# Performance work log

Measured on AMD Instinct MI355X. Metric: run time of the kernel, lower is better.

## Reference

```python
import jax, jax.numpy as jnp
import numpy as np

CONTEXT_SIZE = 2048
CONTEXT_DIM = 1024
HIDDEN_SIZE = 1024
BATCH = 32
SEQLEN = 64


def setup_inputs() -> dict:
    key = jax.random.key(0)
    k1, k2, k3 = jax.random.split(key, 3)
    hidden = jax.random.normal(k1, (1, BATCH, HIDDEN_SIZE), dtype=jnp.float32)
    contextvects = jax.random.normal(k2, (CONTEXT_SIZE, BATCH, CONTEXT_DIM), dtype=jnp.float32)
    # nn.Linear weight: [out_features=context_dim, in_features=hidden_size]
    W = jax.random.normal(k3, (CONTEXT_DIM, HIDDEN_SIZE), dtype=jnp.float32) / np.sqrt(HIDDEN_SIZE)
    padding_mask = jnp.zeros((CONTEXT_SIZE, BATCH), dtype=bool)
    return {"seqlen": SEQLEN, "hidden": hidden, "contextvects": contextvects,
            "W": W, "padding_mask": padding_mask}


def reference(seqlen, hidden, contextvects, W, padding_mask):
    # hidden: [1, B, H] -> [B, H]
    h = hidden[0]
    # Linear projection (no bias): [B, D]
    hidden_proj = h @ W.T
    # scores over context positions: [C, B]
    scores = jnp.einsum('cbd,bd->cb', contextvects, hidden_proj)
    scores = jnp.where(padding_mask, -jnp.inf, scores)
    # softmax over context dim (dim=0)
    attn_weights = jax.nn.softmax(scores, axis=0)  # [C, B]
    # weighted sum of context vectors: [B, D]
    ctx = jnp.einsum('cb,cbd->bd', attn_weights, contextvects)
    # the torch loop recomputes identical values for every step -> broadcast
    context = jnp.broadcast_to(ctx[None], (seqlen, ctx.shape[0], ctx.shape[1]))
    attentions = jnp.broadcast_to(attn_weights.T[None],
                                  (seqlen, attn_weights.shape[1], attn_weights.shape[0]))
    return context, attentions
```

## Files before the change

### kernel.cpp

```cpp
#include <hip/hip_runtime.h>
#include <math.h>

#define C_SIZE 2048
#define D_DIM  1024
#define H_DIM  1024
#define B_SIZE 32
#define S_LEN  64
#define G_NUM  32
#define CG     (C_SIZE / G_NUM)

__global__ __launch_bounds__(256) void hp_kernel(const float* __restrict__ hidden,
                                                 const float* __restrict__ W,
                                                 float* __restrict__ hp) {
    int b    = blockIdx.x;
    int dg   = blockIdx.y;
    int lane = threadIdx.x & 63;
    int wave = threadIdx.x >> 6;

    const float* hrow = hidden + b * H_DIM;
    float4 h4[4];
#pragma unroll
    for (int k = 0; k < 4; ++k) h4[k] = *(const float4*)(hrow + k * 256 + 4 * lane);

    const int d0 = dg * 32 + wave * 8;
    const float* wp = W + (size_t)d0 * H_DIM + 4 * lane;
    float4 wb[2][4];
#pragma unroll
    for (int k = 0; k < 4; ++k) wb[0][k] = *(const float4*)(wp + k * 256);

#pragma unroll
    for (int i = 0; i < 8; ++i) {
        if (i < 7) {
            const float* wn = wp + (size_t)(i + 1) * H_DIM;
#pragma unroll
            for (int k = 0; k < 4; ++k) wb[(i + 1) & 1][k] = *(const float4*)(wn + k * 256);
        }
        float s = 0.f;
#pragma unroll
        for (int k = 0; k < 4; ++k) {
            float4 w4 = wb[i & 1][k];
            s += w4.x * h4[k].x + w4.y * h4[k].y + w4.z * h4[k].z + w4.w * h4[k].w;
        }
        for (int off = 32; off > 0; off >>= 1) s += __shfl_xor(s, off);
        if (lane == 0) hp[b * D_DIM + d0 + i] = s;
    }
}

__global__ __launch_bounds__(256, 4) void fused_kernel(const float* __restrict__ cv,
                                                       const float* __restrict__ hp,
                                                       const unsigned char* __restrict__ mask,
                                                       float* __restrict__ scoresT,
                                                       float* __restrict__ pm,
                                                       float* __restrict__ pl,
                                                       float* __restrict__ pacc) {
    int g    = blockIdx.x;
    int b    = blockIdx.y;
    int lane = threadIdx.x & 63;
    int wave = threadIdx.x >> 6;

    const float* hpb = hp + b * D_DIM;
    float4 hp4[4];
#pragma unroll
    for (int k = 0; k < 4; ++k) hp4[k] = *(const float4*)(hpb + k * 256 + 4 * lane);

    const int    c0      = g * CG + wave * (CG / 4);
    const size_t cstride = (size_t)B_SIZE * D_DIM;
    const float* p0      = cv + ((size_t)c0 * B_SIZE + b) * D_DIM + 4 * lane;

    int mreg = 0;
    if (lane < 16) mreg = mask[(size_t)(c0 + lane) * B_SIZE + b];

    float  m = -3.0e38f, l = 0.f;
    float  myscore = 0.f;
    float4 acc[4];
#pragma unroll
    for (int k = 0; k < 4; ++k) acc[k] = make_float4(0.f, 0.f, 0.f, 0.f);

    float4 buf[2][4];
#pragma unroll
    for (int k = 0; k < 4; ++k) buf[0][k] = *(const float4*)(p0 + k * 256);
#pragma unroll
    for (int k = 0; k < 4; ++k) buf[1][k] = *(const float4*)(p0 + cstride + k * 256);

#pragma unroll
    for (int i = 0; i < 16; ++i) {
        float4 cvv[4];
#pragma unroll
        for (int k = 0; k < 4; ++k) cvv[k] = buf[i & 1][k];

        if (i < 14) {
            const float* pn = p0 + (size_t)(i + 2) * cstride;
#pragma unroll
            for (int k = 0; k < 4; ++k) buf[i & 1][k] = *(const float4*)(pn + k * 256);
        }

        float s = 0.f;
#pragma unroll
        for (int k = 0; k < 4; ++k) {
            s += cvv[k].x * hp4[k].x + cvv[k].y * hp4[k].y +
                 cvv[k].z * hp4[k].z + cvv[k].w * hp4[k].w;
        }
        for (int off = 32; off > 0; off >>= 1) s += __shfl_xor(s, off);

        if (__shfl(mreg, i, 64)) s = -3.0e38f;
        if (lane == i) myscore = s;

        if (s <= m) {
            float p = __expf(s - m);
            l += p;
#pragma unroll
            for (int k = 0; k < 4; ++k) {
                acc[k].x += p * cvv[k].x;
                acc[k].y += p * cvv[k].y;
                acc[k].z += p * cvv[k].z;
                acc[k].w += p * cvv[k].w;
            }
        } else {
            float scale = __expf(m - s);
            l = l * scale + 1.f;
#pragma unroll
            for (int k = 0; k < 4; ++k) {
                acc[k].x = acc[k].x * scale + cvv[k].x;
                acc[k].y = acc[k].y * scale + cvv[k].y;
                acc[k].z = acc[k].z * scale + cvv[k].z;
                acc[k].w = acc[k].w * scale + cvv[k].w;
            }
            m = s;
        }
    }

    if (lane < 16) scoresT[b * C_SIZE + c0 + lane] = myscore;

    __shared__ float sm[4], sl[4];
    __shared__ float accs[4][D_DIM];
    if (lane == 0) { sm[wave] = m; sl[wave] = l; }
    __syncthreads();

    float mb = fmaxf(fmaxf(sm[0], sm[1]), fmaxf(sm[2], sm[3]));
    float myscale = __expf(m - mb);
#pragma unroll
    for (int k = 0; k < 4; ++k) {
        float4 v = acc[k];
        v.x *= myscale; v.y *= myscale; v.z *= myscale; v.w *= myscale;
        *(float4*)&accs[wave][k * 256 + 4 * lane] = v;
    }
    float lb = 0.f;
#pragma unroll
    for (int w = 0; w < 4; ++w) lb += sl[w] * __expf(sm[w] - mb);
    __syncthreads();

    int t = threadIdx.x;
    float4 r = make_float4(0.f, 0.f, 0.f, 0.f);
#pragma unroll
    for (int w = 0; w < 4; ++w) {
        float4 v = *(const float4*)&accs[w][t * 4];
        r.x += v.x; r.y += v.y; r.z += v.z; r.w += v.w;
    }
    *(float4*)(pacc + ((size_t)g * B_SIZE + b) * D_DIM + t * 4) = r;
    if (t == 0) { pm[g * B_SIZE + b] = mb; pl[g * B_SIZE + b] = lb; }
}

__global__ __launch_bounds__(64) void ctx_kernel(const float* __restrict__ pm,
                                                 const float* __restrict__ pl,
                                                 const float* __restrict__ pacc,
                                                 float* __restrict__ Mb,
                                                 float* __restrict__ Lb,
                                                 float* __restrict__ ctxws) {
    int b     = blockIdx.x;
    int dbase = blockIdx.y * 256;
    int lane  = threadIdx.x;

    float mg = (lane < G_NUM) ? pm[lane * B_SIZE + b] : -3.0e38f;
    float M = mg;
    for (int off = 32; off > 0; off >>= 1) M = fmaxf(M, __shfl_xor(M, off));
    float lg = (lane < G_NUM) ? pl[lane * B_SIZE + b] * __expf(mg - M) : 0.f;
    float L = lg;
    for (int off = 32; off > 0; off >>= 1) L += __shfl_xor(L, off);

    __shared__ float ssc[G_NUM];
    if (lane < G_NUM) ssc[lane] = __expf(mg - M);
    __syncthreads();

    float4 r = make_float4(0.f, 0.f, 0.f, 0.f);
#pragma unroll 8
    for (int gi = 0; gi < G_NUM; ++gi) {
        float sc = ssc[gi];
        float4 v = *(const float4*)(pacc + ((size_t)gi * B_SIZE + b) * D_DIM + dbase + 4 * lane);
        r.x += sc * v.x; r.y += sc * v.y; r.z += sc * v.z; r.w += sc * v.w;
    }
    float invL = 1.f / L;
    r.x *= invL; r.y *= invL; r.z *= invL; r.w *= invL;
    *(float4*)(ctxws + b * D_DIM + dbase + 4 * lane) = r;

    if (blockIdx.y == 0 && lane == 0) { Mb[b] = M; Lb[b] = L; }
}

__global__ __launch_bounds__(256) void out_kernel(const float* __restrict__ ctxws,
                                                  const float* __restrict__ scoresT,
                                                  const float* __restrict__ Mb,
                                                  const float* __restrict__ Lb,
                                                  float* __restrict__ out_ctx,
                                                  float* __restrict__ out_attn) {
    int blk = blockIdx.x;
    int b   = blk & (B_SIZE - 1);
    int t   = threadIdx.x;

    float4 cx = *(const float4*)(ctxws + b * D_DIM + t * 4);
    *(float4*)(out_ctx + (size_t)blk * D_DIM + t * 4) = cx;

    float M    = Mb[b];
    float invL = 1.f / Lb[b];
    const float* srow = scoresT + b * C_SIZE;
    float4* orow = (float4*)(out_attn + (size_t)blk * C_SIZE);
#pragma unroll
    for (int k = 0; k < 2; ++k) {
        int c4 = t + k * 256;
        float4 sv = *(const float4*)(srow + c4 * 4);
        float4 av;
        av.x = __expf(sv.x - M) * invL;
        av.y = __expf(sv.y - M) * invL;
        av.z = __expf(sv.z - M) * invL;
        av.w = __expf(sv.w - M) * invL;
        orow[c4] = av;
    }
}

extern "C" void kernel_launch(void* const* d_in, const int* in_sizes, int n_in,
                              void* d_out, int out_size, void* d_ws, size_t ws_size,
                              hipStream_t stream) {
    const float*         hidden = (const float*)d_in[1];
    const float*         cv     = (const float*)d_in[2];
    const float*         W      = (const float*)d_in[3];
    const unsigned char* mask   = (const unsigned char*)d_in[4];

    float* ws = (float*)d_ws;
    float* hp      = ws;
    float* scoresT = ws + 32768;
    float* pm      = ws + 98304;
    float* pl      = ws + 99328;
    float* Mb      = ws + 100352;
    float* Lb      = ws + 100384;
    float* ctxws   = ws + 100416;
    float* pacc    = ws + 133184;

    float* out_ctx  = (float*)d_out;
    float* out_attn = (float*)d_out + (size_t)S_LEN * B_SIZE * D_DIM;

    hp_kernel<<<dim3(B_SIZE, 32), 256, 0, stream>>>(hidden, W, hp);
    fused_kernel<<<dim3(G_NUM, B_SIZE), 256, 0, stream>>>(cv, hp, mask, scoresT, pm, pl, pacc);
    ctx_kernel<<<dim3(B_SIZE, 4), 64, 0, stream>>>(pm, pl, pacc, Mb, Lb, ctxws);
    out_kernel<<<dim3(S_LEN * B_SIZE), 256, 0, stream>>>(ctxws, scoresT, Mb, Lb, out_ctx, out_attn);
}
```

Before: 66.89 us.

## Use 1024-thread blocks with fewer context groups and fold merge into output kernel

The fused attention kernel now runs 16 waves per block over 256 context rows, so the number of partial groups drops from 32 to 8. With only 8 partials, the separate cross-group merge kernel is removed. Each output block recomputes the global max, normalizer and weighted context sum directly from the partials. This removes one launch and the intermediate context buffer, but repeats the small merge in all 2048 output blocks. The grid also shrinks to 256 large blocks with 64KB of shared memory each, which may limit occupancy on the streaming kernel.

```diff
diff --git a/kernel.cpp b/kernel.cpp
--- a/kernel.cpp
+++ b/kernel.cpp
@@ -6,8 +6,7 @@
 #define H_DIM  1024
 #define B_SIZE 32
 #define S_LEN  64
-#define G_NUM  32
-#define CG     (C_SIZE / G_NUM)
+#define G_NUM  8
 
 __global__ __launch_bounds__(256) void hp_kernel(const float* __restrict__ hidden,
                                                  const float* __restrict__ W,
@@ -46,24 +45,25 @@
     }
 }
 
-__global__ __launch_bounds__(256, 4) void fused_kernel(const float* __restrict__ cv,
-                                                       const float* __restrict__ hp,
-                                                       const unsigned char* __restrict__ mask,
-                                                       float* __restrict__ scoresT,
-                                                       float* __restrict__ pm,
-                                                       float* __restrict__ pl,
-                                                       float* __restrict__ pacc) {
+__global__ __launch_bounds__(1024, 4) void fused_kernel(const float* __restrict__ cv,
+                                                        const float* __restrict__ hp,
+                                                        const unsigned char* __restrict__ mask,
+                                                        float* __restrict__ scoresT,
+                                                        float* __restrict__ pm,
+                                                        float* __restrict__ pl,
+                                                        float* __restrict__ pacc) {
     int g    = blockIdx.x;
     int b    = blockIdx.y;
-    int lane = threadIdx.x & 63;
-    int wave = threadIdx.x >> 6;
+    int tid  = threadIdx.x;
+    int lane = tid & 63;
+    int wave = tid >> 6;
 
     const float* hpb = hp + b * D_DIM;
     float4 hp4[4];
 #pragma unroll
     for (int k = 0; k < 4; ++k) hp4[k] = *(const float4*)(hpb + k * 256 + 4 * lane);
 
-    const int    c0      = g * CG + wave * (CG / 4);
+    const int    c0      = g * 256 + wave * 16;
     const size_t cstride = (size_t)B_SIZE * D_DIM;
     const float* p0      = cv + ((size_t)c0 * B_SIZE + b) * D_DIM + 4 * lane;
 
@@ -131,12 +131,15 @@
 
     if (lane < 16) scoresT[b * C_SIZE + c0 + lane] = myscore;
 
-    __shared__ float sm[4], sl[4];
-    __shared__ float accs[4][D_DIM];
+    __shared__ float sm[16], sl[16];
+    __shared__ float accs[16][D_DIM];
     if (lane == 0) { sm[wave] = m; sl[wave] = l; }
     __syncthreads();
 
-    float mb = fmaxf(fmaxf(sm[0], sm[1]), fmaxf(sm[2], sm[3]));
+    float mb = sm[0];
+#pragma unroll
+    for (int w = 1; w < 16; ++w) mb = fmaxf(mb, sm[w]);
+
     float myscale = __expf(m - mb);
 #pragma unroll
     for (int k = 0; k < 4; ++k) {
@@ -146,70 +149,58 @@
     }
     float lb = 0.f;
 #pragma unroll
-    for (int w = 0; w < 4; ++w) lb += sl[w] * __expf(sm[w] - mb);
+    for (int w = 0; w < 16; ++w) lb += sl[w] * __expf(sm[w] - mb);
     __syncthreads();
 
-    int t = threadIdx.x;
+    float r = 0.f;
+#pragma unroll
+    for (int w = 0; w < 16; ++w) r += accs[w][tid];
+    pacc[((size_t)g * B_SIZE + b) * D_DIM + tid] = r;
+    if (tid == 0) { pm[g * B_SIZE + b] = mb; pl[g * B_SIZE + b] = lb; }
+}
+
+__global__ __launch_bounds__(256) void out_kernel(const float* __restrict__ pm,
+                                                  const float* __restrict__ pl,
+                                                  const float* __restrict__ pacc,
+                                                  const float* __restrict__ scoresT,
+                                                  float* __restrict__ out_ctx,
+                                                  float* __restrict__ out_attn) {
+    int blk  = blockIdx.x;
+    int b    = blk & (B_SIZE - 1);
+    int t    = threadIdx.x;
+    int lane = t & 63;
+    int wave = t >> 6;
+
+    __shared__ float ssc[G_NUM];
+    __shared__ float sML[2];
+
+    if (wave == 0) {
+        float mg = (lane < G_NUM) ? pm[lane * B_SIZE + b] : -3.0e38f;
+        float M = mg;
+#pragma unroll
+        for (int off = 4; off > 0; off >>= 1) M = fmaxf(M, __shfl_xor(M, off));
+        float lg = (lane < G_NUM) ? pl[lane * B_SIZE + b] * __expf(mg - M) : 0.f;
+        float L = lg;
+#pragma unroll
+        for (int off = 4; off > 0; off >>= 1) L += __shfl_xor(L, off);
+        if (lane < G_NUM) ssc[lane] = __expf(mg - M);
+        if (lane == 0) { sML[0] = M; sML[1] = L; }
+    }
+    __syncthreads();
+
+    float M    = sML[0];
+    float invL = 1.f / sML[1];
+
     float4 r = make_float4(0.f, 0.f, 0.f, 0.f);
 #pragma unroll
-    for (int w = 0; w < 4; ++w) {
-        float4 v = *(const float4*)&accs[w][t * 4];
-        r.x += v.x; r.y += v.y; r.z += v.z; r.w += v.w;
-    }
-    *(float4*)(pacc + ((size_t)g * B_SIZE + b) * D_DIM + t * 4) = r;
-    if (t == 0) { pm[g * B_SIZE + b] = mb; pl[g * B_SIZE + b] = lb; }
-}
-
-__global__ __launch_bounds__(64) void ctx_kernel(const float* __restrict__ pm,
-                                                 const float* __restrict__ pl,
-                                                 const float* __restrict__ pacc,
-                                                 float* __restrict__ Mb,
-                                                 float* __restrict__ Lb,
-                                                 float* __restrict__ ctxws) {
-    int b     = blockIdx.x;
-    int dbase = blockIdx.y * 256;
-    int lane  = threadIdx.x;
-
-    float mg = (lane < G_NUM) ? pm[lane * B_SIZE + b] : -3.0e38f;
-    float M = mg;
-    for (int off = 32; off > 0; off >>= 1) M = fmaxf(M, __shfl_xor(M, off));
-    float lg = (lane < G_NUM) ? pl[lane * B_SIZE + b] * __expf(mg - M) : 0.f;
-    float L = lg;
-    for (int off = 32; off > 0; off >>= 1) L += __shfl_xor(L, off);
-
-    __shared__ float ssc[G_NUM];
-    if (lane < G_NUM) ssc[lane] = __expf(mg - M);
-    __syncthreads();
-
-    float4 r = make_float4(0.f, 0.f, 0.f, 0.f);
-#pragma unroll 8
     for (int gi = 0; gi < G_NUM; ++gi) {
         float sc = ssc[gi];
-        float4 v = *(const float4*)(pacc + ((size_t)gi * B_SIZE + b) * D_DIM + dbase + 4 * lane);
+        float4 v = *(const float4*)(pacc + ((size_t)gi * B_SIZE + b) * D_DIM + t * 4);
         r.x += sc * v.x; r.y += sc * v.y; r.z += sc * v.z; r.w += sc * v.w;
     }
-    float invL = 1.f / L;
     r.x *= invL; r.y *= invL; r.z *= invL; r.w *= invL;
-    *(float4*)(ctxws + b * D_DIM + dbase + 4 * lane) = r;
-
-    if (blockIdx.y == 0 && lane == 0) { Mb[b] = M; Lb[b] = L; }
-}
-
-__global__ __launch_bounds__(256) void out_kernel(const float* __restrict__ ctxws,
-                                                  const float* __restrict__ scoresT,
-                                                  const float* __restrict__ Mb,
-                                                  const float* __restrict__ Lb,
-                                                  float* __restrict__ out_ctx,
-                                                  float* __restrict__ out_attn) {
-    int blk = blockIdx.x;
-    int b   = blk & (B_SIZE - 1);
-    int t   = threadIdx.x;
-
-    float4 cx = *(const float4*)(ctxws + b * D_DIM + t * 4);
-    *(float4*)(out_ctx + (size_t)blk * D_DIM + t * 4) = cx;
-
-    float M    = Mb[b];
-    float invL = 1.f / Lb[b];
+    *(float4*)(out_ctx + (size_t)blk * D_DIM + t * 4) = r;
+
     const float* srow = scoresT + b * C_SIZE;
     float4* orow = (float4*)(out_attn + (size_t)blk * C_SIZE);
 #pragma unroll
@@ -237,17 +228,13 @@
     float* hp      = ws;
     float* scoresT = ws + 32768;
     float* pm      = ws + 98304;
-    float* pl      = ws + 99328;
-    float* Mb      = ws + 100352;
-    float* Lb      = ws + 100384;
-    float* ctxws   = ws + 100416;
-    float* pacc    = ws + 133184;
+    float* pl      = ws + 98560;
+    float* pacc    = ws + 98816;
 
     float* out_ctx  = (float*)d_out;
     float* out_attn = (float*)d_out + (size_t)S_LEN * B_SIZE * D_DIM;
 
     hp_kernel<<<dim3(B_SIZE, 32), 256, 0, stream>>>(hidden, W, hp);
-    fused_kernel<<<dim3(G_NUM, B_SIZE), 256, 0, stream>>>(cv, hp, mask, scoresT, pm, pl, pacc);
-    ctx_kernel<<<dim3(B_SIZE, 4), 64, 0, stream>>>(pm, pl, pacc, Mb, Lb, ctxws);
-    out_kernel<<<dim3(S_LEN * B_SIZE), 256, 0, stream>>>(ctxws, scoresT, Mb, Lb, out_ctx, out_attn);
-}
+    fused_kernel<<<dim3(G_NUM, B_SIZE), 1024, 0, stream>>>(cv, hp, mask, scoresT, pm, pl, pacc);
+    out_kernel<<<dim3(S_LEN * B_SIZE), 256, 0, stream>>>(pm, pl, pacc, scoresT, out_ctx, out_attn);
+}
```

Measured after the change: 64.56 us. 3.5% less time.
